# Performance work log

Measured on AMD Instinct MI355X. Metric: run time of the kernel, lower is better.

## Reference

```python
import jax, jax.numpy as jnp
import numpy as np

SCALE_REACH = 10.0   # 'scale' in forward
SCALE_COS = 16.0     # CosNorm_Classifier default scale


def setup_inputs() -> dict:
    key = jax.random.key(0)
    ks = jax.random.split(key, 7)
    B, C, F = 64, 1000, 2048
    return {
        "x": jax.random.normal(ks[0], (B, F), jnp.float32),
        "centroids": jax.random.normal(ks[1], (C, F), jnp.float32),
        "W_hall": jax.random.normal(ks[2], (C, F), jnp.float32) * 0.02,
        "b_hall": jax.random.normal(ks[3], (C,), jnp.float32) * 0.02,
        "W_sel": jax.random.normal(ks[4], (F, F), jnp.float32) * 0.02,
        "b_sel": jax.random.normal(ks[5], (F,), jnp.float32) * 0.02,
        "W_cos": jax.random.normal(ks[6], (C, F), jnp.float32) * 0.001,
    }


def reference(x, centroids, W_hall, b_hall, W_sel, b_sel, W_cos):
    direct_feature = x
    # L2 distance to every class centroid: [B, C] (materializes [B, C, F] diff as in torch)
    diff = x[:, None, :] - centroids[None, :, :]
    dist = jnp.sqrt(jnp.sum(diff * diff, axis=2))
    # original sorts then takes column 0 -> min distance
    min_dist = jnp.min(dist, axis=1)                      # [B]
    reachability = (SCALE_REACH / min_dist)[:, None]      # [B, 1], broadcast over feat

    # hallucinated memory read
    values_memory = jax.nn.softmax(x @ W_hall.T + b_hall, axis=1)  # [B, C]
    memory_feature = values_memory @ centroids                      # [B, F]

    concept_selector = jnp.tanh(x @ W_sel.T + b_sel)                # [B, F]
    infused_feature = concept_selector * memory_feature
    feat = reachability * (direct_feature + infused_feature)

    # CosNorm classifier
    norm_x = jnp.linalg.norm(feat, axis=1, keepdims=True)           # [B, 1]
    ex = (norm_x / (1.0 + norm_x)) * (feat / norm_x)                # norm-gated unit vec
    ew = W_cos / jnp.linalg.norm(W_cos, axis=1, keepdims=True)      # [C, F]
    logits = ex @ (ew.T * SCALE_COS)                                # [B, C]

    return logits, direct_feature, infused_feature
```

## Files before the change

kernel.cpp:

```cpp
#include <hip/hip_runtime.h>
#include <math.h>

#define BB 64
#define CC 1000
#define FF 2048
#define KB 32

#define OFF_SPART 0
#define OFF_HPART 1024000
#define OFF_SELP  2048000
#define OFF_MEMP  3096576
#define OFF_LOGP  4145152
#define OFF_V     5169152
#define OFF_FEAT  5233152
#define OFF_CN2   5364224
#define OFF_WINV  5365224
#define OFF_XN2   5366224
#define OFF_REACH 5366288
#define OFF_SFAC  5366352

__device__ __forceinline__ void stage_bt(const float* __restrict__ M, int ldK, int rowBase,
                                         int nrows, int k0, int kmax, float* Ts, int t) {
  int r = t >> 2;
  int q = t & 3;
  int grow = rowBase + r;
  bool rok = grow < nrows;
  const float* src = M + (size_t)grow * ldK + k0 + q * 8;
#pragma unroll
  for (int h = 0; h < 2; ++h) {
    int kbase = q * 8 + h * 4;
    float4 v = make_float4(0.f, 0.f, 0.f, 0.f);
    if (rok) {
      if (k0 + kbase + 3 < kmax) {
        v = *(const float4*)(src + h * 4);
      } else {
#pragma unroll
        for (int j = 0; j < 4; ++j) {
          int kk = k0 + kbase + j;
          if (kk < kmax) ((float*)&v)[j] = src[h * 4 + j];
        }
      }
    }
    Ts[(kbase + 0) * 64 + r] = v.x;
    Ts[(kbase + 1) * 64 + r] = v.y;
    Ts[(kbase + 2) * 64 + r] = v.z;
    Ts[(kbase + 3) * 64 + r] = v.w;
  }
}

__device__ __forceinline__ void stage_bn(const float* __restrict__ M, int ldN, int k0, int kmax,
                                         int n0, float* Ts, int t) {
  int kk = t >> 3;
  int c8 = (t & 7) * 8;
  int gk = k0 + kk;
  const float* src = M + (size_t)gk * ldN + n0 + c8;
#pragma unroll
  for (int h = 0; h < 2; ++h) {
    float4 v = make_float4(0.f, 0.f, 0.f, 0.f);
    if (gk < kmax) v = *(const float4*)(src + h * 4);
    *(float4*)(Ts + kk * 64 + c8 + h * 4) = v;
  }
}

__global__ __launch_bounds__(256) void k_phase1(
    const float* __restrict__ x, const float* __restrict__ cent,
    const float* __restrict__ whall, const float* __restrict__ wsel,
    const float* __restrict__ wcos, float* __restrict__ ws) {
  __shared__ float lds[3 * KB * 64];
  float* As = lds;
  float* B1s = lds + KB * 64;
  float* B2s = lds + 2 * KB * 64;
  int bx = blockIdx.x;
  int t = threadIdx.x;
  int tx = t & 15, ty = t >> 4;

  if (bx < 256) {
    int tile = bx & 15, ks = bx >> 4;
    int n0 = tile * 64;
    float accS[4][4] = {{0.f}}, accH[4][4] = {{0.f}};
    for (int kc = 0; kc < 128; kc += KB) {
      int k0 = ks * 128 + kc;
      __syncthreads();
      stage_bt(x, FF, 0, BB, k0, FF, As, t);
      stage_bt(cent, FF, n0, CC, k0, FF, B1s, t);
      stage_bt(whall, FF, n0, CC, k0, FF, B2s, t);
      __syncthreads();
#pragma unroll 8
      for (int kk = 0; kk < KB; ++kk) {
        float4 av = *(const float4*)(As + kk * 64 + ty * 4);
        float4 b1 = *(const float4*)(B1s + kk * 64 + tx * 4);
        float4 b2 = *(const float4*)(B2s + kk * 64 + tx * 4);
        float a[4] = {av.x, av.y, av.z, av.w};
        float p[4] = {b1.x, b1.y, b1.z, b1.w};
        float q2[4] = {b2.x, b2.y, b2.z, b2.w};
#pragma unroll
        for (int i = 0; i < 4; ++i)
#pragma unroll
          for (int j = 0; j < 4; ++j) {
            accS[i][j] += a[i] * p[j];
            accH[i][j] += a[i] * q2[j];
          }
      }
    }
    float* Spart = ws + OFF_SPART;
    float* Hpart = ws + OFF_HPART;
#pragma unroll
    for (int i = 0; i < 4; ++i) {
      int row = ty * 4 + i;
      size_t base = ((size_t)ks * 64 + row) * 1000;
      int n = n0 + tx * 4;
      if (n + 3 < 1000) {
        *(float4*)(Spart + base + n) = make_float4(accS[i][0], accS[i][1], accS[i][2], accS[i][3]);
        *(float4*)(Hpart + base + n) = make_float4(accH[i][0], accH[i][1], accH[i][2], accH[i][3]);
      } else {
        for (int j = 0; j < 4; ++j)
          if (n + j < 1000) { Spart[base + n + j] = accS[i][j]; Hpart[base + n + j] = accH[i][j]; }
      }
    }
  } else if (bx < 512) {
    int b2i = bx - 256;
    int tile = b2i & 31, ks = b2i >> 5;
    int n0 = tile * 64;
    float acc[4][4] = {{0.f}};
    for (int kc = 0; kc < 256; kc += KB) {
      int k0 = ks * 256 + kc;
      __syncthreads();
      stage_bt(x, FF, 0, BB, k0, FF, As, t);
      stage_bt(wsel, FF, n0, FF, k0, FF, B1s, t);
      __syncthreads();
#pragma unroll 8
      for (int kk = 0; kk < KB; ++kk) {
        float4 av = *(const float4*)(As + kk * 64 + ty * 4);
        float4 b1 = *(const float4*)(B1s + kk * 64 + tx * 4);
        float a[4] = {av.x, av.y, av.z, av.w};
        float p[4] = {b1.x, b1.y, b1.z, b1.w};
#pragma unroll
        for (int i = 0; i < 4; ++i)
#pragma unroll
          for (int j = 0; j < 4; ++j) acc[i][j] += a[i] * p[j];
      }
    }
    float* selp = ws + OFF_SELP;
#pragma unroll
    for (int i = 0; i < 4; ++i) {
      int row = ty * 4 + i;
      size_t base = ((size_t)ks * 64 + row) * 2048;
      int n = n0 + tx * 4;
      *(float4*)(selp + base + n) = make_float4(acc[i][0], acc[i][1], acc[i][2], acc[i][3]);
    }
  } else {
    int nb = bx - 512;
    int w = t >> 6, lane = t & 63;
    int r = nb * 4 + w;
    const float* src;
    if (r < 1000) src = cent + (size_t)r * FF;
    else if (r < 2000) src = wcos + (size_t)(r - 1000) * FF;
    else src = x + (size_t)(r - 2000) * FF;
    float s = 0.f;
#pragma unroll
    for (int i = 0; i < 8; ++i) {
      float4 v = *(const float4*)(src + i * 256 + lane * 4);
      s += v.x * v.x + v.y * v.y + v.z * v.z + v.w * v.w;
    }
#pragma unroll
    for (int off = 32; off > 0; off >>= 1) s += __shfl_down(s, off, 64);
    if (lane == 0) {
      if (r < 1000) ws[OFF_CN2 + r] = s;
      else if (r < 2000) ws[OFF_WINV + (r - 1000)] = 1.f / sqrtf(s);
      else ws[OFF_XN2 + (r - 2000)] = s;
    }
  }
}

__global__ __launch_bounds__(256) void k_softmax(const float* __restrict__ bhall,
                                                 float* __restrict__ ws) {
  int b = blockIdx.x, t = threadIdx.x;
  const float* Spart = ws + OFF_SPART;
  const float* Hpart = ws + OFF_HPART;
  __shared__ float hrow[1000];
  __shared__ float red[256];
  float xn = ws[OFF_XN2 + b];
  float lmin = 3.0e38f, lmax = -3.0e38f;
  for (int c = t; c < 1000; c += 256) {
    float S = 0.f, H = 0.f;
#pragma unroll
    for (int ks = 0; ks < 16; ++ks) {
      S += Spart[(size_t)ks * 64000 + b * 1000 + c];
      H += Hpart[(size_t)ks * 64000 + b * 1000 + c];
    }
    H += bhall[c];
    hrow[c] = H;
    float d2 = xn - 2.f * S + ws[OFF_CN2 + c];
    lmin = fminf(lmin, d2);
    lmax = fmaxf(lmax, H);
  }
  red[t] = lmin; __syncthreads();
  for (int s = 128; s > 0; s >>= 1) { if (t < s) red[t] = fminf(red[t], red[t + s]); __syncthreads(); }
  float bmin = red[0]; __syncthreads();
  red[t] = lmax; __syncthreads();
  for (int s = 128; s > 0; s >>= 1) { if (t < s) red[t] = fmaxf(red[t], red[t + s]); __syncthreads(); }
  float bmax = red[0]; __syncthreads();
  float lsum = 0.f;
  for (int c = t; c < 1000; c += 256) {
    float e = expf(hrow[c] - bmax);
    hrow[c] = e;
    lsum += e;
  }
  red[t] = lsum; __syncthreads();
  for (int s = 128; s > 0; s >>= 1) { if (t < s) red[t] += red[t + s]; __syncthreads(); }
  float inv = 1.f / red[0];
  float* V = ws + OFF_V;
  for (int c = t; c < 1000; c += 256) V[b * 1000 + c] = hrow[c] * inv;
  if (t == 0) ws[OFF_REACH + b] = 10.f / sqrtf(bmin);
}

__global__ __launch_bounds__(256) void k_mem(const float* __restrict__ cent,
                                             float* __restrict__ ws) {
  __shared__ float As[KB * 64];
  __shared__ float Bs[KB * 64];
  int bx = blockIdx.x, t = threadIdx.x;
  int tile = bx & 31, ks = bx >> 5;
  int n0 = tile * 64;
  int tx = t & 15, ty = t >> 4;
  const float* V = ws + OFF_V;
  float acc[4][4] = {{0.f}};
  for (int kc = 0; kc < 128; kc += KB) {
    int k0 = ks * 128 + kc;
    __syncthreads();
    stage_bt(V, 1000, 0, BB, k0, 1000, As, t);
    stage_bn(cent, FF, k0, 1000, n0, Bs, t);
    __syncthreads();
#pragma unroll 8
    for (int kk = 0; kk < KB; ++kk) {
      float4 av = *(const float4*)(As + kk * 64 + ty * 4);
      float4 bv = *(const float4*)(Bs + kk * 64 + tx * 4);
      float a[4] = {av.x, av.y, av.z, av.w};
      float p[4] = {bv.x, bv.y, bv.z, bv.w};
#pragma unroll
      for (int i = 0; i < 4; ++i)
#pragma unroll
        for (int j = 0; j < 4; ++j) acc[i][j] += a[i] * p[j];
    }
  }
  float* memp = ws + OFF_MEMP;
#pragma unroll
  for (int i = 0; i < 4; ++i) {
    size_t base = ((size_t)ks * 64 + ty * 4 + i) * 2048;
    int n = n0 + tx * 4;
    *(float4*)(memp + base + n) = make_float4(acc[i][0], acc[i][1], acc[i][2], acc[i][3]);
  }
}

__global__ __launch_bounds__(256) void k_fuse(const float* __restrict__ x,
                                              const float* __restrict__ bsel,
                                              float* __restrict__ ws, float* __restrict__ out) {
  int b = blockIdx.x, t = threadIdx.x;
  const float* selp = ws + OFF_SELP;
  const float* memp = ws + OFF_MEMP;
  float rch = ws[OFF_REACH + b];
  __shared__ float red[256];
  float nrm2 = 0.f;
  float* feat = ws + OFF_FEAT;
  for (int f = t; f < 2048; f += 256) {
    float sp = bsel[f], mm = 0.f;
#pragma unroll
    for (int ks = 0; ks < 8; ++ks) {
      sp += selp[(size_t)ks * 131072 + b * 2048 + f];
      mm += memp[(size_t)ks * 131072 + b * 2048 + f];
    }
    float sel = tanhf(sp);
    float inf = sel * mm;
    float xv = x[b * 2048 + f];
    float ft = rch * (xv + inf);
    out[64000 + b * 2048 + f] = xv;
    out[195072 + b * 2048 + f] = inf;
    feat[b * 2048 + f] = ft;
    nrm2 += ft * ft;
  }
  red[t] = nrm2; __syncthreads();
  for (int s = 128; s > 0; s >>= 1) { if (t < s) red[t] += red[t + s]; __syncthreads(); }
  if (t == 0) ws[OFF_SFAC + b] = 16.f / (1.f + sqrtf(red[0]));
}

__global__ __launch_bounds__(256) void k_loggemm(const float* __restrict__ wcos,
                                                 float* __restrict__ ws) {
  __shared__ float As[KB * 64];
  __shared__ float Bs[KB * 64];
  int bx = blockIdx.x, t = threadIdx.x;
  int tile = bx & 15, ks = bx >> 4;
  int n0 = tile * 64;
  int tx = t & 15, ty = t >> 4;
  const float* feat = ws + OFF_FEAT;
  float acc[4][4] = {{0.f}};
  for (int kc = 0; kc < 128; kc += KB) {
    int k0 = ks * 128 + kc;
    __syncthreads();
    stage_bt(feat, FF, 0, BB, k0, FF, As, t);
    stage_bt(wcos, FF, n0, CC, k0, FF, Bs, t);
    __syncthreads();
#pragma unroll 8
    for (int kk = 0; kk < KB; ++kk) {
      float4 av = *(const float4*)(As + kk * 64 + ty * 4);
      float4 bv = *(const float4*)(Bs + kk * 64 + tx * 4);
      float a[4] = {av.x, av.y, av.z, av.w};
      float p[4] = {bv.x, bv.y, bv.z, bv.w};
#pragma unroll
      for (int i = 0; i < 4; ++i)
#pragma unroll
        for (int j = 0; j < 4; ++j) acc[i][j] += a[i] * p[j];
    }
  }
  float* logp = ws + OFF_LOGP;
#pragma unroll
  for (int i = 0; i < 4; ++i) {
    size_t base = ((size_t)ks * 64 + ty * 4 + i) * 1000;
    int n = n0 + tx * 4;
    if (n + 3 < 1000) {
      *(float4*)(logp + base + n) = make_float4(acc[i][0], acc[i][1], acc[i][2], acc[i][3]);
    } else {
      for (int j = 0; j < 4; ++j)
        if (n + j < 1000) logp[base + n + j] = acc[i][j];
    }
  }
}

__global__ __launch_bounds__(256) void k_final(float* __restrict__ ws, float* __restrict__ out) {
  int idx = blockIdx.x * 256 + threadIdx.x;
  if (idx >= 64000) return;
  const float* logp = ws + OFF_LOGP;
  float s = 0.f;
#pragma unroll
  for (int ks = 0; ks < 16; ++ks) s += logp[(size_t)ks * 64000 + idx];
  int b = idx / 1000;
  int c = idx - b * 1000;
  out[idx] = s * ws[OFF_SFAC + b] * ws[OFF_WINV + c];
}

extern "C" void kernel_launch(void* const* d_in, const int* in_sizes, int n_in,
                              void* d_out, int out_size, void* d_ws, size_t ws_size,
                              hipStream_t stream) {
  const float* x     = (const float*)d_in[0];
  const float* cent  = (const float*)d_in[1];
  const float* whall = (const float*)d_in[2];
  const float* bhall = (const float*)d_in[3];
  const float* wsel  = (const float*)d_in[4];
  const float* bsel  = (const float*)d_in[5];
  const float* wcos  = (const float*)d_in[6];
  float* out = (float*)d_out;
  float* ws  = (float*)d_ws;

  hipLaunchKernelGGL(k_phase1, dim3(1028), dim3(256), 0, stream, x, cent, whall, wsel, wcos, ws);
  hipLaunchKernelGGL(k_softmax, dim3(64), dim3(256), 0, stream, bhall, ws);
  hipLaunchKernelGGL(k_mem, dim3(256), dim3(256), 0, stream, cent, ws);
  hipLaunchKernelGGL(k_fuse, dim3(64), dim3(256), 0, stream, x, bsel, ws, out);
  hipLaunchKernelGGL(k_loggemm, dim3(256), dim3(256), 0, stream, wcos, ws);
  hipLaunchKernelGGL(k_final, dim3(250), dim3(256), 0, stream, ws, out);
}
```

Measured before the change: 148.4 us.

## Use split-bf16 MFMA matrix cores for all GEMMs instead of scalar FP32 FMA

```diff
diff --git a/kernel.cpp b/kernel.cpp
--- a/kernel.cpp
+++ b/kernel.cpp
@@ -1,156 +1,205 @@
 #include <hip/hip_runtime.h>
 #include <math.h>
 
-#define BB 64
-#define CC 1000
 #define FF 2048
-#define KB 32
+
+typedef __attribute__((ext_vector_type(8))) short short8;
+typedef __attribute__((ext_vector_type(4))) float floatx4;
 
 #define OFF_SPART 0
-#define OFF_HPART 1024000
-#define OFF_SELP  2048000
-#define OFF_MEMP  3096576
-#define OFF_LOGP  4145152
-#define OFF_V     5169152
-#define OFF_FEAT  5233152
-#define OFF_CN2   5364224
-#define OFF_WINV  5365224
-#define OFF_XN2   5366224
-#define OFF_REACH 5366288
-#define OFF_SFAC  5366352
-
-__device__ __forceinline__ void stage_bt(const float* __restrict__ M, int ldK, int rowBase,
-                                         int nrows, int k0, int kmax, float* Ts, int t) {
-  int r = t >> 2;
-  int q = t & 3;
+#define OFF_HPART 512000
+#define OFF_SELP  1024000
+#define OFF_MEMP  2072576
+#define OFF_LOGP  3121152
+#define OFF_V     3633152
+#define OFF_FEAT  3697152
+#define OFF_CN2   3828224
+#define OFF_WINV  3829224
+#define OFF_XN2   3830224
+#define OFF_REACH 3830288
+#define OFF_SFAC  3830352
+
+#define TP 40
+
+__device__ __forceinline__ void split2(float f, ushort& h, ushort& l) {
+  unsigned u = __float_as_uint(f);
+  float r = f - __uint_as_float(u & 0xffff0000u);
+  h = (ushort)(u >> 16);
+  l = (ushort)(__float_as_uint(r) >> 16);
+}
+
+__device__ __forceinline__ void stage_bt_bf(const float* __restrict__ M, int ldK, int rowBase,
+                                            int nrows, int k0, int kmax,
+                                            ushort* __restrict__ hi, ushort* __restrict__ lo, int t) {
+  int r = t >> 2, q = t & 3;
   int grow = rowBase + r;
   bool rok = grow < nrows;
   const float* src = M + (size_t)grow * ldK + k0 + q * 8;
 #pragma unroll
   for (int h = 0; h < 2; ++h) {
-    int kbase = q * 8 + h * 4;
+    int kb = k0 + q * 8 + h * 4;
     float4 v = make_float4(0.f, 0.f, 0.f, 0.f);
     if (rok) {
-      if (k0 + kbase + 3 < kmax) {
+      if (kb + 3 < kmax) {
         v = *(const float4*)(src + h * 4);
       } else {
 #pragma unroll
-        for (int j = 0; j < 4; ++j) {
-          int kk = k0 + kbase + j;
-          if (kk < kmax) ((float*)&v)[j] = src[h * 4 + j];
-        }
-      }
-    }
-    Ts[(kbase + 0) * 64 + r] = v.x;
-    Ts[(kbase + 1) * 64 + r] = v.y;
-    Ts[(kbase + 2) * 64 + r] = v.z;
-    Ts[(kbase + 3) * 64 + r] = v.w;
-  }
-}
-
-__device__ __forceinline__ void stage_bn(const float* __restrict__ M, int ldN, int k0, int kmax,
-                                         int n0, float* Ts, int t) {
-  int kk = t >> 3;
-  int c8 = (t & 7) * 8;
+        for (int j = 0; j < 4; ++j)
+          if (kb + j < kmax) ((float*)&v)[j] = src[h * 4 + j];
+      }
+    }
+    ushort4 hv, lv;
+    split2(v.x, hv.x, lv.x); split2(v.y, hv.y, lv.y);
+    split2(v.z, hv.z, lv.z); split2(v.w, hv.w, lv.w);
+    int base = r * TP + q * 8 + h * 4;
+    *(ushort4*)(hi + base) = hv;
+    *(ushort4*)(lo + base) = lv;
+  }
+}
+
+__device__ __forceinline__ void stage_tr_bf(const float* __restrict__ M, int ldN, int k0, int kmax,
+                                            int n0, ushort* __restrict__ hi, ushort* __restrict__ lo, int t) {
+  int kk = t >> 3, c8 = (t & 7) * 8;
   int gk = k0 + kk;
   const float* src = M + (size_t)gk * ldN + n0 + c8;
-#pragma unroll
-  for (int h = 0; h < 2; ++h) {
-    float4 v = make_float4(0.f, 0.f, 0.f, 0.f);
-    if (gk < kmax) v = *(const float4*)(src + h * 4);
-    *(float4*)(Ts + kk * 64 + c8 + h * 4) = v;
-  }
-}
+  float4 v0 = make_float4(0.f, 0.f, 0.f, 0.f), v1 = v0;
+  if (gk < kmax) { v0 = *(const float4*)src; v1 = *(const float4*)(src + 4); }
+#pragma unroll
+  for (int j = 0; j < 8; ++j) {
+    float f = (j < 4) ? ((float*)&v0)[j] : ((float*)&v1)[j - 4];
+    ushort h, l;
+    split2(f, h, l);
+    hi[(c8 + j) * TP + kk] = h;
+    lo[(c8 + j) * TP + kk] = l;
+  }
+}
+
+#define MFMA(a, b, c) __builtin_amdgcn_mfma_f32_16x16x32_bf16(a, b, c, 0, 0, 0)
 
 __global__ __launch_bounds__(256) void k_phase1(
     const float* __restrict__ x, const float* __restrict__ cent,
     const float* __restrict__ whall, const float* __restrict__ wsel,
     const float* __restrict__ wcos, float* __restrict__ ws) {
-  __shared__ float lds[3 * KB * 64];
-  float* As = lds;
-  float* B1s = lds + KB * 64;
-  float* B2s = lds + 2 * KB * 64;
-  int bx = blockIdx.x;
-  int t = threadIdx.x;
-  int tx = t & 15, ty = t >> 4;
-
-  if (bx < 256) {
+  __shared__ ushort u_lds[6 * 64 * TP];
+  ushort* Ah  = u_lds;
+  ushort* Al  = u_lds + 64 * TP;
+  ushort* B1h = u_lds + 2 * 64 * TP;
+  ushort* B1l = u_lds + 3 * 64 * TP;
+  ushort* B2h = u_lds + 4 * 64 * TP;
+  ushort* B2l = u_lds + 5 * 64 * TP;
+  int bx = blockIdx.x, t = threadIdx.x;
+  int ln15 = t & 15;
+  int lq = (t >> 4) & 3;
+  int q8 = lq * 8;
+  int w = t >> 6;
+  int mh = w & 1, nh = w >> 1;
+
+  if (bx < 128) {
     int tile = bx & 15, ks = bx >> 4;
     int n0 = tile * 64;
-    float accS[4][4] = {{0.f}}, accH[4][4] = {{0.f}};
-    for (int kc = 0; kc < 128; kc += KB) {
-      int k0 = ks * 128 + kc;
+    floatx4 accS[2][2], accH[2][2];
+#pragma unroll
+    for (int i = 0; i < 2; ++i)
+#pragma unroll
+      for (int j = 0; j < 2; ++j) { accS[i][j] = (floatx4){0.f,0.f,0.f,0.f}; accH[i][j] = (floatx4){0.f,0.f,0.f,0.f}; }
+    for (int kc = 0; kc < 8; ++kc) {
+      int k0 = ks * 256 + kc * 32;
       __syncthreads();
-      stage_bt(x, FF, 0, BB, k0, FF, As, t);
-      stage_bt(cent, FF, n0, CC, k0, FF, B1s, t);
-      stage_bt(whall, FF, n0, CC, k0, FF, B2s, t);
+      stage_bt_bf(x,     FF, 0,  64,   k0, FF, Ah,  Al,  t);
+      stage_bt_bf(cent,  FF, n0, 1000, k0, FF, B1h, B1l, t);
+      stage_bt_bf(whall, FF, n0, 1000, k0, FF, B2h, B2l, t);
       __syncthreads();
-#pragma unroll 8
-      for (int kk = 0; kk < KB; ++kk) {
-        float4 av = *(const float4*)(As + kk * 64 + ty * 4);
-        float4 b1 = *(const float4*)(B1s + kk * 64 + tx * 4);
-        float4 b2 = *(const float4*)(B2s + kk * 64 + tx * 4);
-        float a[4] = {av.x, av.y, av.z, av.w};
-        float p[4] = {b1.x, b1.y, b1.z, b1.w};
-        float q2[4] = {b2.x, b2.y, b2.z, b2.w};
-#pragma unroll
-        for (int i = 0; i < 4; ++i)
-#pragma unroll
-          for (int j = 0; j < 4; ++j) {
-            accS[i][j] += a[i] * p[j];
-            accH[i][j] += a[i] * q2[j];
+      short8 ah[2], al[2];
+#pragma unroll
+      for (int i = 0; i < 2; ++i) {
+        int row = (mh * 2 + i) * 16 + ln15;
+        ah[i] = *(const short8*)(Ah + row * TP + q8);
+        al[i] = *(const short8*)(Al + row * TP + q8);
+      }
+#pragma unroll
+      for (int j = 0; j < 2; ++j) {
+        int brow = (nh * 2 + j) * 16 + ln15;
+        short8 b1h = *(const short8*)(B1h + brow * TP + q8);
+        short8 b1l = *(const short8*)(B1l + brow * TP + q8);
+        short8 b2h = *(const short8*)(B2h + brow * TP + q8);
+        short8 b2l = *(const short8*)(B2l + brow * TP + q8);
+#pragma unroll
+        for (int i = 0; i < 2; ++i) {
+          accS[i][j] = MFMA(ah[i], b1h, accS[i][j]);
+          accS[i][j] = MFMA(ah[i], b1l, accS[i][j]);
+          accS[i][j] = MFMA(al[i], b1h, accS[i][j]);
+          accH[i][j] = MFMA(ah[i], b2h, accH[i][j]);
+          accH[i][j] = MFMA(ah[i], b2l, accH[i][j]);
+          accH[i][j] = MFMA(al[i], b2h, accH[i][j]);
+        }
+      }
+    }
+    float* Spart = ws + OFF_SPART + (size_t)ks * 64000;
+    float* Hpart = ws + OFF_HPART + (size_t)ks * 64000;
+#pragma unroll
+    for (int i = 0; i < 2; ++i)
+#pragma unroll
+      for (int j = 0; j < 2; ++j) {
+        int gn = n0 + (nh * 2 + j) * 16 + ln15;
+        if (gn < 1000) {
+#pragma unroll
+          for (int r = 0; r < 4; ++r) {
+            int gm = (mh * 2 + i) * 16 + lq * 4 + r;
+            Spart[gm * 1000 + gn] = accS[i][j][r];
+            Hpart[gm * 1000 + gn] = accH[i][j][r];
           }
-      }
-    }
-    float* Spart = ws + OFF_SPART;
-    float* Hpart = ws + OFF_HPART;
-#pragma unroll
-    for (int i = 0; i < 4; ++i) {
-      int row = ty * 4 + i;
-      size_t base = ((size_t)ks * 64 + row) * 1000;
-      int n = n0 + tx * 4;
-      if (n + 3 < 1000) {
-        *(float4*)(Spart + base + n) = make_float4(accS[i][0], accS[i][1], accS[i][2], accS[i][3]);
-        *(float4*)(Hpart + base + n) = make_float4(accH[i][0], accH[i][1], accH[i][2], accH[i][3]);
-      } else {
-        for (int j = 0; j < 4; ++j)
-          if (n + j < 1000) { Spart[base + n + j] = accS[i][j]; Hpart[base + n + j] = accH[i][j]; }
-      }
-    }
-  } else if (bx < 512) {
-    int b2i = bx - 256;
-    int tile = b2i & 31, ks = b2i >> 5;
+        }
+      }
+  } else if (bx < 384) {
+    int b2 = bx - 128;
+    int tile = b2 & 31, ks = b2 >> 5;
     int n0 = tile * 64;
-    float acc[4][4] = {{0.f}};
-    for (int kc = 0; kc < 256; kc += KB) {
-      int k0 = ks * 256 + kc;
+    floatx4 acc[2][2];
+#pragma unroll
+    for (int i = 0; i < 2; ++i)
+#pragma unroll
+      for (int j = 0; j < 2; ++j) acc[i][j] = (floatx4){0.f,0.f,0.f,0.f};
+    for (int kc = 0; kc < 8; ++kc) {
+      int k0 = ks * 256 + kc * 32;
       __syncthreads();
-      stage_bt(x, FF, 0, BB, k0, FF, As, t);
-      stage_bt(wsel, FF, n0, FF, k0, FF, B1s, t);
+      stage_bt_bf(x,    FF, 0,  64,  k0, FF, Ah,  Al,  t);
+      stage_bt_bf(wsel, FF, n0, FF,  k0, FF, B1h, B1l, t);
       __syncthreads();
-#pragma unroll 8
-      for (int kk = 0; kk < KB; ++kk) {
-        float4 av = *(const float4*)(As + kk * 64 + ty * 4);
-        float4 b1 = *(const float4*)(B1s + kk * 64 + tx * 4);
-        float a[4] = {av.x, av.y, av.z, av.w};
-        float p[4] = {b1.x, b1.y, b1.z, b1.w};
-#pragma unroll
-        for (int i = 0; i < 4; ++i)
-#pragma unroll
-          for (int j = 0; j < 4; ++j) acc[i][j] += a[i] * p[j];
-      }
-    }
-    float* selp = ws + OFF_SELP;
-#pragma unroll
-    for (int i = 0; i < 4; ++i) {
-      int row = ty * 4 + i;
-      size_t base = ((size_t)ks * 64 + row) * 2048;
-      int n = n0 + tx * 4;
-      *(float4*)(selp + base + n) = make_float4(acc[i][0], acc[i][1], acc[i][2], acc[i][3]);
-    }
+      short8 ah[2], al[2];
+#pragma unroll
+      for (int i = 0; i < 2; ++i) {
+        int row = (mh * 2 + i) * 16 + ln15;
+        ah[i] = *(const short8*)(Ah + row * TP + q8);
+        al[i] = *(const short8*)(Al + row * TP + q8);
+      }
+#pragma unroll
+      for (int j = 0; j < 2; ++j) {
+        int brow = (nh * 2 + j) * 16 + ln15;
+        short8 bh = *(const short8*)(B1h + brow * TP + q8);
+        short8 bl = *(const short8*)(B1l + brow * TP + q8);
+#pragma unroll
+        for (int i = 0; i < 2; ++i) {
+          acc[i][j] = MFMA(ah[i], bh, acc[i][j]);
+          acc[i][j] = MFMA(ah[i], bl, acc[i][j]);
+          acc[i][j] = MFMA(al[i], bh, acc[i][j]);
+        }
+      }
+    }
+    float* selp = ws + OFF_SELP + (size_t)ks * 131072;
+#pragma unroll
+    for (int i = 0; i < 2; ++i)
+#pragma unroll
+      for (int j = 0; j < 2; ++j) {
+        int gn = n0 + (nh * 2 + j) * 16 + ln15;
+#pragma unroll
+        for (int r = 0; r < 4; ++r) {
+          int gm = (mh * 2 + i) * 16 + lq * 4 + r;
+          selp[gm * 2048 + gn] = acc[i][j][r];
+        }
+      }
   } else {
-    int nb = bx - 512;
-    int w = t >> 6, lane = t & 63;
+    int nb = bx - 384;
+    int lane = t & 63;
     int r = nb * 4 + w;
     const float* src;
     if (r < 1000) src = cent + (size_t)r * FF;
@@ -184,7 +233,7 @@
   for (int c = t; c < 1000; c += 256) {
     float S = 0.f, H = 0.f;
 #pragma unroll
-    for (int ks = 0; ks < 16; ++ks) {
+    for (int ks = 0; ks < 8; ++ks) {
       S += Spart[(size_t)ks * 64000 + b * 1000 + c];
       H += Hpart[(size_t)ks * 64000 + b * 1000 + c];
     }
@@ -216,39 +265,60 @@
 
 __global__ __launch_bounds__(256) void k_mem(const float* __restrict__ cent,
                                              float* __restrict__ ws) {
-  __shared__ float As[KB * 64];
-  __shared__ float Bs[KB * 64];
+  __shared__ ushort u_lds[4 * 64 * TP];
+  ushort* Ah = u_lds;
+  ushort* Al = u_lds + 64 * TP;
+  ushort* Bh = u_lds + 2 * 64 * TP;
+  ushort* Bl = u_lds + 3 * 64 * TP;
   int bx = blockIdx.x, t = threadIdx.x;
   int tile = bx & 31, ks = bx >> 5;
   int n0 = tile * 64;
-  int tx = t & 15, ty = t >> 4;
+  int ln15 = t & 15, lq = (t >> 4) & 3, q8 = lq * 8;
+  int w = t >> 6, mh = w & 1, nh = w >> 1;
   const float* V = ws + OFF_V;
-  float acc[4][4] = {{0.f}};
-  for (int kc = 0; kc < 128; kc += KB) {
-    int k0 = ks * 128 + kc;
+  floatx4 acc[2][2];
+#pragma unroll
+  for (int i = 0; i < 2; ++i)
+#pragma unroll
+    for (int j = 0; j < 2; ++j) acc[i][j] = (floatx4){0.f,0.f,0.f,0.f};
+  for (int kc = 0; kc < 4; ++kc) {
+    int k0 = ks * 128 + kc * 32;
     __syncthreads();
-    stage_bt(V, 1000, 0, BB, k0, 1000, As, t);
-    stage_bn(cent, FF, k0, 1000, n0, Bs, t);
+    stage_bt_bf(V, 1000, 0, 64, k0, 1000, Ah, Al, t);
+    stage_tr_bf(cent, FF, k0, 1000, n0, Bh, Bl, t);
     __syncthreads();
-#pragma unroll 8
-    for (int kk = 0; kk < KB; ++kk) {
-      float4 av = *(const float4*)(As + kk * 64 + ty * 4);
-      float4 bv = *(const float4*)(Bs + kk * 64 + tx * 4);
-      float a[4] = {av.x, av.y, av.z, av.w};
-      float p[4] = {bv.x, bv.y, bv.z, bv.w};
-#pragma unroll
-      for (int i = 0; i < 4; ++i)
-#pragma unroll
-        for (int j = 0; j < 4; ++j) acc[i][j] += a[i] * p[j];
-    }
-  }
-  float* memp = ws + OFF_MEMP;
-#pragma unroll
-  for (int i = 0; i < 4; ++i) {
-    size_t base = ((size_t)ks * 64 + ty * 4 + i) * 2048;
-    int n = n0 + tx * 4;
-    *(float4*)(memp + base + n) = make_float4(acc[i][0], acc[i][1], acc[i][2], acc[i][3]);
-  }
+    short8 ah[2], al[2];
+#pragma unroll
+    for (int i = 0; i < 2; ++i) {
+      int row = (mh * 2 + i) * 16 + ln15;
+      ah[i] = *(const short8*)(Ah + row * TP + q8);
+      al[i] = *(const short8*)(Al + row * TP + q8);
+    }
+#pragma unroll
+    for (int j = 0; j < 2; ++j) {
+      int brow = (nh * 2 + j) * 16 + ln15;
+      short8 bh = *(const short8*)(Bh + brow * TP + q8);
+      short8 bl = *(const short8*)(Bl + brow * TP + q8);
+#pragma unroll
+      for (int i = 0; i < 2; ++i) {
+        acc[i][j] = MFMA(ah[i], bh, acc[i][j]);
+        acc[i][j] = MFMA(ah[i], bl, acc[i][j]);
+        acc[i][j] = MFMA(al[i], bh, acc[i][j]);
+      }
+    }
+  }
+  float* memp = ws + OFF_MEMP + (size_t)ks * 131072;
+#pragma unroll
+  for (int i = 0; i < 2; ++i)
+#pragma unroll
+    for (int j = 0; j < 2; ++j) {
+      int gn = n0 + (nh * 2 + j) * 16 + ln15;
+#pragma unroll
+      for (int r = 0; r < 4; ++r) {
+        int gm = (mh * 2 + i) * 16 + lq * 4 + r;
+        memp[gm * 2048 + gn] = acc[i][j][r];
+      }
+    }
 }
 
 __global__ __launch_bounds__(256) void k_fuse(const float* __restrict__ x,
@@ -284,44 +354,62 @@
 
 __global__ __launch_bounds__(256) void k_loggemm(const float* __restrict__ wcos,
                                                  float* __restrict__ ws) {
-  __shared__ float As[KB * 64];
-  __shared__ float Bs[KB * 64];
+  __shared__ ushort u_lds[4 * 64 * TP];
+  ushort* Ah = u_lds;
+  ushort* Al = u_lds + 64 * TP;
+  ushort* Bh = u_lds + 2 * 64 * TP;
+  ushort* Bl = u_lds + 3 * 64 * TP;
   int bx = blockIdx.x, t = threadIdx.x;
   int tile = bx & 15, ks = bx >> 4;
   int n0 = tile * 64;
-  int tx = t & 15, ty = t >> 4;
+  int ln15 = t & 15, lq = (t >> 4) & 3, q8 = lq * 8;
+  int w = t >> 6, mh = w & 1, nh = w >> 1;
   const float* feat = ws + OFF_FEAT;
-  float acc[4][4] = {{0.f}};
-  for (int kc = 0; kc < 128; kc += KB) {
-    int k0 = ks * 128 + kc;
+  floatx4 acc[2][2];
+#pragma unroll
+  for (int i = 0; i < 2; ++i)
+#pragma unroll
+    for (int j = 0; j < 2; ++j) acc[i][j] = (floatx4){0.f,0.f,0.f,0.f};
+  for (int kc = 0; kc < 8; ++kc) {
+    int k0 = ks * 256 + kc * 32;
     __syncthreads();
-    stage_bt(feat, FF, 0, BB, k0, FF, As, t);
-    stage_bt(wcos, FF, n0, CC, k0, FF, Bs, t);
+    stage_bt_bf(feat, FF, 0,  64,   k0, FF, Ah, Al, t);
+    stage_bt_bf(wcos, FF, n0, 1000, k0, FF, Bh, Bl, t);
     __syncthreads();
-#pragma unroll 8
-    for (int kk = 0; kk < KB; ++kk) {
-      float4 av = *(const float4*)(As + kk * 64 + ty * 4);
-      float4 bv = *(const float4*)(Bs + kk * 64 + tx * 4);
-      float a[4] = {av.x, av.y, av.z, av.w};
-      float p[4] = {bv.x, bv.y, bv.z, bv.w};
-#pragma unroll
-      for (int i = 0; i < 4; ++i)
-#pragma unroll
-        for (int j = 0; j < 4; ++j) acc[i][j] += a[i] * p[j];
-    }
-  }
-  float* logp = ws + OFF_LOGP;
-#pragma unroll
-  for (int i = 0; i < 4; ++i) {
-    size_t base = ((size_t)ks * 64 + ty * 4 + i) * 1000;
-    int n = n0 + tx * 4;
-    if (n + 3 < 1000) {
-      *(float4*)(logp + base + n) = make_float4(acc[i][0], acc[i][1], acc[i][2], acc[i][3]);
-    } else {
-      for (int j = 0; j < 4; ++j)
-        if (n + j < 1000) logp[base + n + j] = acc[i][j];
-    }
-  }
+    short8 ah[2], al[2];
+#pragma unroll
+    for (int i = 0; i < 2; ++i) {
+      int row = (mh * 2 + i) * 16 + ln15;
+      ah[i] = *(const short8*)(Ah + row * TP + q8);
+      al[i] = *(const short8*)(Al + row * TP + q8);
+    }
+#pragma unroll
+    for (int j = 0; j < 2; ++j) {
+      int brow = (nh * 2 + j) * 16 + ln15;
+      short8 bh = *(const short8*)(Bh + brow * TP + q8);
+      short8 bl = *(const short8*)(Bl + brow * TP + q8);
+#pragma unroll
+      for (int i = 0; i < 2; ++i) {
+        acc[i][j] = MFMA(ah[i], bh, acc[i][j]);
+        acc[i][j] = MFMA(ah[i], bl, acc[i][j]);
+        acc[i][j] = MFMA(al[i], bh, acc[i][j]);
+      }
+    }
+  }
+  float* logp = ws + OFF_LOGP + (size_t)ks * 64000;
+#pragma unroll
+  for (int i = 0; i < 2; ++i)
+#pragma unroll
+    for (int j = 0; j < 2; ++j) {
+      int gn = n0 + (nh * 2 + j) * 16 + ln15;
+      if (gn < 1000) {
+#pragma unroll
+        for (int r = 0; r < 4; ++r) {
+          int gm = (mh * 2 + i) * 16 + lq * 4 + r;
+          logp[gm * 1000 + gn] = acc[i][j][r];
+        }
+      }
+    }
 }
 
 __global__ __launch_bounds__(256) void k_final(float* __restrict__ ws, float* __restrict__ out) {
@@ -330,7 +418,7 @@
   const float* logp = ws + OFF_LOGP;
   float s = 0.f;
 #pragma unroll
-  for (int ks = 0; ks < 16; ++ks) s += logp[(size_t)ks * 64000 + idx];
+  for (int ks = 0; ks < 8; ++ks) s += logp[(size_t)ks * 64000 + idx];
   int b = idx / 1000;
   int c = idx - b * 1000;
   out[idx] = s * ws[OFF_SFAC + b] * ws[OFF_WINV + c];
@@ -349,10 +437,10 @@
   float* out = (float*)d_out;
   float* ws  = (float*)d_ws;
 
-  hipLaunchKernelGGL(k_phase1, dim3(1028), dim3(256), 0, stream, x, cent, whall, wsel, wcos, ws);
+  hipLaunchKernelGGL(k_phase1, dim3(900), dim3(256), 0, stream, x, cent, whall, wsel, wcos, ws);
   hipLaunchKernelGGL(k_softmax, dim3(64), dim3(256), 0, stream, bhall, ws);
   hipLaunchKernelGGL(k_mem, dim3(256), dim3(256), 0, stream, cent, ws);
   hipLaunchKernelGGL(k_fuse, dim3(64), dim3(256), 0, stream, x, bsel, ws, out);
-  hipLaunchKernelGGL(k_loggemm, dim3(256), dim3(256), 0, stream, wcos, ws);
+  hipLaunchKernelGGL(k_loggemm, dim3(128), dim3(256), 0, stream, wcos, ws);
   hipLaunchKernelGGL(k_final, dim3(250), dim3(256), 0, stream, ws, out);
 }
```

Result: faster. 144.4 us (-2.7%).
